# Performance work log

Hardware: AMD Instinct MI355X
Metric: run time of the kernel (lower is better)

Reference implementation:

```python
import jax, jax.numpy as jnp
import numpy as np

BATCH = 16384
D_MODEL = 2048
N_EXPERT = 64


def setup_inputs() -> dict:
    key = jax.random.key(0)
    kx, kw = jax.random.split(key)
    x = jax.random.normal(kx, (BATCH, D_MODEL), dtype=jnp.float32)
    # nn.Linear(d_model, n_expert, bias=False) -> weight [n_expert, d_model]
    w_gate = jax.random.normal(kw, (N_EXPERT, D_MODEL), dtype=jnp.float32) * (1.0 / np.sqrt(D_MODEL))
    return {"x": x, "w_gate": w_gate}


def reference(x, w_gate):
    # logits = x @ W^T : [batch, n_expert]
    logits = jnp.einsum("bd,ed->be", x, w_gate)
    idx = jnp.argmax(logits, axis=-1)                       # [batch]
    mask = jax.nn.one_hot(idx, logits.shape[-1], dtype=jnp.float32)  # [batch, nE]
    scores = jnp.sum(mask * logits, axis=-1, keepdims=True)  # [batch, 1]
    return (idx, scores, mask)
```

## Files before the change

kernel.cpp:

```cpp
#include <hip/hip_runtime.h>


typedef float  f32x4  __attribute__((ext_vector_type(4)));
typedef short  bf16x8 __attribute__((ext_vector_type(8)));

constexpr int BATCH = 16384;
constexpr int DM    = 2048;
constexpr int NE    = 64;
constexpr int BM    = 32;
constexpr int NT    = 256;


__device__ __forceinline__ void split_bf16(float f, unsigned short& hi, unsigned short& lo) {
    unsigned u  = __float_as_uint(f);
    unsigned h  = (u + 0x8000u) >> 16;
    float    hf = __uint_as_float(h << 16);
    unsigned l  = __float_as_uint(f - hf) >> 16;
    hi = (unsigned short)h;
    lo = (unsigned short)l;
}

__global__ __launch_bounds__(256, 1)
void wconv_kernel(const float* __restrict__ w, unsigned short* __restrict__ wf) {
    int i  = blockIdx.x * 256 + threadIdx.x;
    int ks = i >> 11;
    int n  = (i >> 9) & 3;
    int l  = (i >> 3) & 63;
    int j  = i & 7;
    int e  = n * 16 + (l & 15);
    int k  = ks * 32 + (l >> 4) * 8 + j;
    float v = w[(size_t)e * DM + k];
    unsigned short hi, lo;
    split_bf16(v, hi, lo);
    int base = ((ks * 2 + 0) * 4 + n) * 512 + l * 8 + j;
    wf[base]        = hi;
    wf[base + 2048] = lo;
}

struct BSet  { bf16x8 v[8]; };
struct BPair { BSet a, b; };

#define WAITV(N) do { asm volatile("s_waitcnt vmcnt(" #N ")" ::: "memory"); \
                      __builtin_amdgcn_sched_barrier(0); } while (0)
#define BARR     do { __builtin_amdgcn_sched_barrier(0); \
                      __builtin_amdgcn_s_barrier(); \
                      __builtin_amdgcn_sched_barrier(0); } while (0)

__global__ __launch_bounds__(NT, 2)
void gate_kernel(const float* __restrict__ x,
                 const unsigned short* __restrict__ wf,
                 float* __restrict__ out) {
    __shared__ alignas(16) float xs[4][16 * 64 * 4];
    __shared__ float lg[BM][NE + 1];
    __shared__ int   s_idx[BM];

    const int t     = threadIdx.x;
    const int lane  = t & 63;
    const int q     = t >> 6;
    const int row0  = blockIdx.x * BM;
    const int phase = blockIdx.x & 7;

    f32x4 acc[2][4];
    #pragma unroll
    for (int h = 0; h < 2; ++h)
        #pragma unroll
        for (int n = 0; n < 4; ++n) acc[h][n] = (f32x4){0.f, 0.f, 0.f, 0.f};

    auto sph = [&](int ss) { return (ss + phase) & 7; };

    auto stage_x = [&](int c) {
        const int h = c & 1;
        const float* xg = x + (size_t)(row0 + h * 16) * DM + sph(c >> 1) * 256;
        float* dst = &xs[c & 3][0];
        #pragma unroll
        for (int i = 0; i < 4; ++i) {
            int d  = i * NT + t;
            int r  = d >> 6;
            int sd = d & 63;
            int sr = sd ^ (r & 7);
            __builtin_amdgcn_global_load_lds(
                (const __attribute__((address_space(1))) void*)(xg + (size_t)r * DM + sr * 4),
                (__attribute__((address_space(3))) void*)(dst + d * 4),
                16, 0, 0);
        }
    };

    auto load_bs = [&](int ks, BSet& B) {
        const unsigned short* wg = wf + (size_t)ks * 4096 + lane * 8;
        #pragma unroll
        for (int f = 0; f < 8; ++f)
            B.v[f] = *(const bf16x8*)(wg + (size_t)f * 512);
    };
    auto load_pair = [&](int ss, BPair& P) {
        int base = sph(ss) * 8 + q * 2;
        load_bs(base + 0, P.a);
        load_bs(base + 1, P.b);
    };

    auto compute = [&](int c, int hh, const BPair& P) {
        const float* src = &xs[c & 3][0];
        const int rA = lane & 15;
        const int xr = rA & 7;
        #pragma unroll
        for (int kk = 0; kk < 2; ++kk) {
            const BSet& B = kk ? P.b : P.a;
            const int c0 = q * 16 + kk * 8 + ((lane >> 4) << 1);
            f32x4 a0 = *(const f32x4*)(src + (rA * 64 + ((c0 + 0) ^ xr)) * 4);
            f32x4 a1 = *(const f32x4*)(src + (rA * 64 + ((c0 + 1) ^ xr)) * 4);
            bf16x8 ahi, alo;
            #pragma unroll
            for (int j = 0; j < 8; ++j) {
                float f = (j < 4) ? a0[j] : a1[j - 4];
                unsigned short h, l;
                split_bf16(f, h, l);
                ahi[j] = (short)h;
                alo[j] = (short)l;
            }
            #pragma unroll
            for (int n = 0; n < 4; ++n) {
                acc[hh][n] = __builtin_amdgcn_mfma_f32_16x16x32_bf16(ahi, B.v[0 + n], acc[hh][n], 0, 0, 0);
                acc[hh][n] = __builtin_amdgcn_mfma_f32_16x16x32_bf16(ahi, B.v[4 + n], acc[hh][n], 0, 0, 0);
                acc[hh][n] = __builtin_amdgcn_mfma_f32_16x16x32_bf16(alo, B.v[0 + n], acc[hh][n], 0, 0, 0);
            }
        }
    };

    BPair PA, PB;

    load_pair(0, PA);
    stage_x(0);
    stage_x(1);

    #pragma unroll 1
    for (int ss = 0; ss < 6; ss += 2) {
        const int c = 2 * ss;
        load_pair(ss + 1, PB);
        stage_x(c + 2);
        WAITV(24); BARR;
        compute(c + 0, 0, PA);
        stage_x(c + 3);
        WAITV(24); BARR;
        compute(c + 1, 1, PA);
        load_pair(ss + 2, PA);
        stage_x(c + 4);
        WAITV(24); BARR;
        compute(c + 2, 0, PB);
        stage_x(c + 5);
        WAITV(24); BARR;
        compute(c + 3, 1, PB);
    }
    load_pair(7, PB);
    stage_x(14);
    WAITV(24); BARR;
    compute(12, 0, PA);
    stage_x(15);
    WAITV(24); BARR;
    compute(13, 1, PA);
    WAITV(4);  BARR;
    compute(14, 0, PB);
    WAITV(0);  BARR;
    compute(15, 1, PB);
    __syncthreads();

    const int rb = (lane >> 4) << 2;
    const int cb = lane & 15;
    if (q == 0) {
        #pragma unroll
        for (int h = 0; h < 2; ++h)
            #pragma unroll
            for (int n = 0; n < 4; ++n)
                #pragma unroll
                for (int j = 0; j < 4; ++j)
                    lg[h * 16 + rb + j][n * 16 + cb] = acc[h][n][j];
    }
    __syncthreads();
    if (q == 1) {
        #pragma unroll
        for (int h = 0; h < 2; ++h)
            #pragma unroll
            for (int n = 0; n < 4; ++n)
                #pragma unroll
                for (int j = 0; j < 4; ++j)
                    lg[h * 16 + rb + j][n * 16 + cb] += acc[h][n][j];
    }
    __syncthreads();
    if (q == 2) {
        #pragma unroll
        for (int h = 0; h < 2; ++h)
            #pragma unroll
            for (int n = 0; n < 4; ++n)
                #pragma unroll
                for (int j = 0; j < 4; ++j)
                    lg[h * 16 + rb + j][n * 16 + cb] += acc[h][n][j];
    }
    __syncthreads();
    if (q == 3) {
        #pragma unroll
        for (int h = 0; h < 2; ++h)
            #pragma unroll
            for (int n = 0; n < 4; ++n)
                #pragma unroll
                for (int j = 0; j < 4; ++j)
                    lg[h * 16 + rb + j][n * 16 + cb] += acc[h][n][j];
    }
    __syncthreads();

    if (t < BM) {
        float m  = lg[t][0];
        int   mi = 0;
        #pragma unroll
        for (int e = 1; e < NE; ++e) {
            float v = lg[t][e];
            if (v > m) { m = v; mi = e; }
        }
        s_idx[t] = mi;
        out[row0 + t]         = (float)mi;
        out[BATCH + row0 + t] = m;
    }
    __syncthreads();

    float* mask = out + 2 * (size_t)BATCH;
    int r  = t >> 3;
    int c0 = (t & 7) * 8;
    int mi = s_idx[r];
    #pragma unroll
    for (int i = 0; i < 2; ++i) {
        f32x4 v;
        #pragma unroll
        for (int j = 0; j < 4; ++j) v[j] = (c0 + i * 4 + j == mi) ? 1.0f : 0.0f;
        *(f32x4*)&mask[(size_t)(row0 + r) * NE + c0 + i * 4] = v;
    }
}

extern "C" void kernel_launch(void* const* d_in, const int* in_sizes, int n_in,
                              void* d_out, int out_size, void* d_ws, size_t ws_size,
                              hipStream_t stream) {
    const float* x = (const float*)d_in[0];
    const float* w = (const float*)d_in[1];
    float* out     = (float*)d_out;
    unsigned short* wf = (unsigned short*)d_ws;

    wconv_kernel<<<dim3(512), dim3(256), 0, stream>>>(w, wf);
    gate_kernel<<<dim3(BATCH / BM), dim3(NT), 0, stream>>>(x, wf, out);
}
```

Before: 43.65 us.

## Fuse weight bf16 split into gate kernel via LDS staging of fp32 weights

Drops the separate weight-conversion kernel and launch. Each block now streams fp32 weight tiles into LDS with async global-to-LDS loads and does the hi/lo bf16 split in registers before the MFMAs. The K step is halved to 128 and the pipeline is rebuilt around 16 stages with weight and x staging per pair. The cost is redundant weight conversion in every block, extra LDS traffic, and more barriers per K step.

```diff
diff --git a/kernel.cpp b/kernel.cpp
--- a/kernel.cpp
+++ b/kernel.cpp
@@ -9,7 +9,6 @@
 constexpr int NE    = 64;
 constexpr int BM    = 32;
 constexpr int NT    = 256;
-
 
 __device__ __forceinline__ void split_bf16(float f, unsigned short& hi, unsigned short& lo) {
     unsigned u  = __float_as_uint(f);
@@ -20,25 +19,7 @@
     lo = (unsigned short)l;
 }
 
-__global__ __launch_bounds__(256, 1)
-void wconv_kernel(const float* __restrict__ w, unsigned short* __restrict__ wf) {
-    int i  = blockIdx.x * 256 + threadIdx.x;
-    int ks = i >> 11;
-    int n  = (i >> 9) & 3;
-    int l  = (i >> 3) & 63;
-    int j  = i & 7;
-    int e  = n * 16 + (l & 15);
-    int k  = ks * 32 + (l >> 4) * 8 + j;
-    float v = w[(size_t)e * DM + k];
-    unsigned short hi, lo;
-    split_bf16(v, hi, lo);
-    int base = ((ks * 2 + 0) * 4 + n) * 512 + l * 8 + j;
-    wf[base]        = hi;
-    wf[base + 2048] = lo;
-}
-
-struct BSet  { bf16x8 v[8]; };
-struct BPair { BSet a, b; };
+struct BSet { bf16x8 v[8]; };
 
 #define WAITV(N) do { asm volatile("s_waitcnt vmcnt(" #N ")" ::: "memory"); \
                       __builtin_amdgcn_sched_barrier(0); } while (0)
@@ -48,9 +29,10 @@
 
 __global__ __launch_bounds__(NT, 2)
 void gate_kernel(const float* __restrict__ x,
-                 const unsigned short* __restrict__ wf,
+                 const float* __restrict__ w,
                  float* __restrict__ out) {
-    __shared__ alignas(16) float xs[4][16 * 64 * 4];
+    __shared__ alignas(16) float xs[4][16 * 32 * 4];
+    __shared__ alignas(16) float ws4[64 * 32 * 4];
     __shared__ float lg[BM][NE + 1];
     __shared__ int   s_idx[BM];
 
@@ -58,7 +40,7 @@
     const int lane  = t & 63;
     const int q     = t >> 6;
     const int row0  = blockIdx.x * BM;
-    const int phase = blockIdx.x & 7;
+    const int phase = blockIdx.x & 15;
 
     f32x4 acc[2][4];
     #pragma unroll
@@ -66,17 +48,17 @@
         #pragma unroll
         for (int n = 0; n < 4; ++n) acc[h][n] = (f32x4){0.f, 0.f, 0.f, 0.f};
 
-    auto sph = [&](int ss) { return (ss + phase) & 7; };
+    auto kb = [&](int p) { return (p + phase) & 15; };
 
     auto stage_x = [&](int c) {
         const int h = c & 1;
-        const float* xg = x + (size_t)(row0 + h * 16) * DM + sph(c >> 1) * 256;
+        const float* xg = x + (size_t)(row0 + h * 16) * DM + kb(c >> 1) * 128;
         float* dst = &xs[c & 3][0];
         #pragma unroll
-        for (int i = 0; i < 4; ++i) {
+        for (int i = 0; i < 2; ++i) {
             int d  = i * NT + t;
-            int r  = d >> 6;
-            int sd = d & 63;
+            int r  = d >> 5;
+            int sd = d & 31;
             int sr = sd ^ (r & 7);
             __builtin_amdgcn_global_load_lds(
                 (const __attribute__((address_space(1))) void*)(xg + (size_t)r * DM + sr * 4),
@@ -85,81 +67,93 @@
         }
     };
 
-    auto load_bs = [&](int ks, BSet& B) {
-        const unsigned short* wg = wf + (size_t)ks * 4096 + lane * 8;
-        #pragma unroll
-        for (int f = 0; f < 8; ++f)
-            B.v[f] = *(const bf16x8*)(wg + (size_t)f * 512);
-    };
-    auto load_pair = [&](int ss, BPair& P) {
-        int base = sph(ss) * 8 + q * 2;
-        load_bs(base + 0, P.a);
-        load_bs(base + 1, P.b);
-    };
-
-    auto compute = [&](int c, int hh, const BPair& P) {
+    auto stage_w = [&](int p) {
+        const float* wg = w + (size_t)kb(p) * 128;
+        #pragma unroll
+        for (int i = 0; i < 8; ++i) {
+            int d  = i * NT + t;
+            int e  = d >> 5;
+            int sd = d & 31;
+            int sr = sd ^ (e & 7);
+            __builtin_amdgcn_global_load_lds(
+                (const __attribute__((address_space(1))) void*)(wg + (size_t)e * DM + sr * 4),
+                (__attribute__((address_space(3))) void*)(ws4 + d * 4),
+                16, 0, 0);
+        }
+    };
+
+    auto compute = [&](int c, int hh, const BSet& B) {
         const float* src = &xs[c & 3][0];
         const int rA = lane & 15;
-        const int xr = rA & 7;
-        #pragma unroll
-        for (int kk = 0; kk < 2; ++kk) {
-            const BSet& B = kk ? P.b : P.a;
-            const int c0 = q * 16 + kk * 8 + ((lane >> 4) << 1);
-            f32x4 a0 = *(const f32x4*)(src + (rA * 64 + ((c0 + 0) ^ xr)) * 4);
-            f32x4 a1 = *(const f32x4*)(src + (rA * 64 + ((c0 + 1) ^ xr)) * 4);
-            bf16x8 ahi, alo;
+        const int s0 = q * 8 + ((lane >> 4) << 1);
+        f32x4 a0 = *(const f32x4*)(src + (size_t)(rA * 32 + ((s0 + 0) ^ (rA & 7))) * 4);
+        f32x4 a1 = *(const f32x4*)(src + (size_t)(rA * 32 + ((s0 + 1) ^ (rA & 7))) * 4);
+        bf16x8 ahi, alo;
+        #pragma unroll
+        for (int j = 0; j < 8; ++j) {
+            float f = (j < 4) ? a0[j] : a1[j - 4];
+            unsigned short h, l;
+            split_bf16(f, h, l);
+            ahi[j] = (short)h;
+            alo[j] = (short)l;
+        }
+        #pragma unroll
+        for (int n = 0; n < 4; ++n) {
+            acc[hh][n] = __builtin_amdgcn_mfma_f32_16x16x32_bf16(ahi, B.v[0 + n], acc[hh][n], 0, 0, 0);
+            acc[hh][n] = __builtin_amdgcn_mfma_f32_16x16x32_bf16(ahi, B.v[4 + n], acc[hh][n], 0, 0, 0);
+            acc[hh][n] = __builtin_amdgcn_mfma_f32_16x16x32_bf16(alo, B.v[0 + n], acc[hh][n], 0, 0, 0);
+        }
+    };
+
+    auto pairbody = [&](int p) {
+        BSet S;
+        #pragma unroll
+        for (int n = 0; n < 4; ++n) {
+            const int e  = n * 16 + (lane & 15);
+            const int s0 = q * 8 + ((lane >> 4) << 1);
+            f32x4 w0 = *(const f32x4*)&ws4[(size_t)(e * 32 + ((s0 + 0) ^ (e & 7))) * 4];
+            f32x4 w1 = *(const f32x4*)&ws4[(size_t)(e * 32 + ((s0 + 1) ^ (e & 7))) * 4];
+            bf16x8 hi8, lo8;
             #pragma unroll
             for (int j = 0; j < 8; ++j) {
-                float f = (j < 4) ? a0[j] : a1[j - 4];
+                float f = (j < 4) ? w0[j] : w1[j - 4];
                 unsigned short h, l;
                 split_bf16(f, h, l);
-                ahi[j] = (short)h;
-                alo[j] = (short)l;
+                hi8[j] = (short)h;
+                lo8[j] = (short)l;
             }
-            #pragma unroll
-            for (int n = 0; n < 4; ++n) {
-                acc[hh][n] = __builtin_amdgcn_mfma_f32_16x16x32_bf16(ahi, B.v[0 + n], acc[hh][n], 0, 0, 0);
-                acc[hh][n] = __builtin_amdgcn_mfma_f32_16x16x32_bf16(ahi, B.v[4 + n], acc[hh][n], 0, 0, 0);
-                acc[hh][n] = __builtin_amdgcn_mfma_f32_16x16x32_bf16(alo, B.v[0 + n], acc[hh][n], 0, 0, 0);
-            }
-        }
-    };
-
-    BPair PA, PB;
-
-    load_pair(0, PA);
+            S.v[n]     = hi8;
+            S.v[4 + n] = lo8;
+        }
+        compute(2 * p + 0, 0, S);
+        compute(2 * p + 1, 1, S);
+    };
+
     stage_x(0);
     stage_x(1);
+    stage_w(0);
+    stage_x(2);
+    stage_x(3);
+    WAITV(4);
+    BARR;
+    pairbody(0);
 
     #pragma unroll 1
-    for (int ss = 0; ss < 6; ss += 2) {
-        const int c = 2 * ss;
-        load_pair(ss + 1, PB);
-        stage_x(c + 2);
-        WAITV(24); BARR;
-        compute(c + 0, 0, PA);
-        stage_x(c + 3);
-        WAITV(24); BARR;
-        compute(c + 1, 1, PA);
-        load_pair(ss + 2, PA);
-        stage_x(c + 4);
-        WAITV(24); BARR;
-        compute(c + 2, 0, PB);
-        stage_x(c + 5);
-        WAITV(24); BARR;
-        compute(c + 3, 1, PB);
-    }
-    load_pair(7, PB);
-    stage_x(14);
-    WAITV(24); BARR;
-    compute(12, 0, PA);
-    stage_x(15);
-    WAITV(24); BARR;
-    compute(13, 1, PA);
-    WAITV(4);  BARR;
-    compute(14, 0, PB);
-    WAITV(0);  BARR;
-    compute(15, 1, PB);
+    for (int p = 1; p < 15; ++p) {
+        BARR;
+        stage_w(p);
+        stage_x(2 * p + 2);
+        stage_x(2 * p + 3);
+        WAITV(4);
+        BARR;
+        pairbody(p);
+    }
+
+    BARR;
+    stage_w(15);
+    WAITV(0);
+    BARR;
+    pairbody(15);
     __syncthreads();
 
     const int rb = (lane >> 4) << 2;
@@ -238,8 +232,6 @@
     const float* x = (const float*)d_in[0];
     const float* w = (const float*)d_in[1];
     float* out     = (float*)d_out;
-    unsigned short* wf = (unsigned short*)d_ws;
-
-    wconv_kernel<<<dim3(512), dim3(256), 0, stream>>>(w, wf);
-    gate_kernel<<<dim3(BATCH / BM), dim3(NT), 0, stream>>>(x, wf, out);
+
+    gate_kernel<<<dim3(BATCH / BM), dim3(NT), 0, stream>>>(x, w, out);
 }
```

Measured after the change: 38.56 us. 1.13x faster.

## Stage gate weights through LDS and double the row tile to 64

Applied to the files above, without the earlier changes.

The block tile grows to 64 rows with 512 threads. Each of the two row-tiles of waves splits K four ways. The bf16 hi/lo weight slab is now copied into LDS with global_load_lds and shared by all waves, instead of each wave holding B fragments in registers from global loads. The pipeline becomes a simple double-buffered loop over 16 K-chunks, each staging both x and the weights. The aim is to halve weight traffic per row and cut register pressure, at the cost of fewer resident blocks, extra LDS reads for B and a barrier-heavy two-stage pipeline.

```diff
diff --git a/kernel.cpp b/kernel.cpp
--- a/kernel.cpp
+++ b/kernel.cpp
@@ -7,8 +7,9 @@
 constexpr int BATCH = 16384;
 constexpr int DM    = 2048;
 constexpr int NE    = 64;
-constexpr int BM    = 32;
-constexpr int NT    = 256;
+constexpr int BM    = 64;
+constexpr int NT    = 512;
+constexpr int NCH   = 16;
 
 
 __device__ __forceinline__ void split_bf16(float f, unsigned short& hi, unsigned short& lo) {
@@ -37,46 +38,45 @@
     wf[base + 2048] = lo;
 }
 
-struct BSet  { bf16x8 v[8]; };
-struct BPair { BSet a, b; };
-
 #define WAITV(N) do { asm volatile("s_waitcnt vmcnt(" #N ")" ::: "memory"); \
                       __builtin_amdgcn_sched_barrier(0); } while (0)
 #define BARR     do { __builtin_amdgcn_sched_barrier(0); \
                       __builtin_amdgcn_s_barrier(); \
                       __builtin_amdgcn_sched_barrier(0); } while (0)
 
-__global__ __launch_bounds__(NT, 2)
+__global__ __launch_bounds__(NT, 1)
 void gate_kernel(const float* __restrict__ x,
                  const unsigned short* __restrict__ wf,
                  float* __restrict__ out) {
-    __shared__ alignas(16) float xs[4][16 * 64 * 4];
+    __shared__ alignas(16) float          xs[2][BM * 32 * 4];
+    __shared__ alignas(16) unsigned short bs[2][4 * 4096];
     __shared__ float lg[BM][NE + 1];
     __shared__ int   s_idx[BM];
 
     const int t     = threadIdx.x;
     const int lane  = t & 63;
-    const int q     = t >> 6;
+    const int wv    = t >> 6;
+    const int rt    = wv >> 2;
+    const int q     = wv & 3;
     const int row0  = blockIdx.x * BM;
-    const int phase = blockIdx.x & 7;
+    const int phase = blockIdx.x & 15;
 
     f32x4 acc[2][4];
     #pragma unroll
-    for (int h = 0; h < 2; ++h)
-        #pragma unroll
-        for (int n = 0; n < 4; ++n) acc[h][n] = (f32x4){0.f, 0.f, 0.f, 0.f};
-
-    auto sph = [&](int ss) { return (ss + phase) & 7; };
+    for (int s = 0; s < 2; ++s)
+        #pragma unroll
+        for (int n = 0; n < 4; ++n) acc[s][n] = (f32x4){0.f, 0.f, 0.f, 0.f};
+
+    auto ckOf = [&](int c) { return (c + phase) & 15; };
 
     auto stage_x = [&](int c) {
-        const int h = c & 1;
-        const float* xg = x + (size_t)(row0 + h * 16) * DM + sph(c >> 1) * 256;
-        float* dst = &xs[c & 3][0];
+        const float* xg = x + (size_t)row0 * DM + ckOf(c) * 128;
+        float* dst = &xs[c & 1][0];
         #pragma unroll
         for (int i = 0; i < 4; ++i) {
             int d  = i * NT + t;
-            int r  = d >> 6;
-            int sd = d & 63;
+            int r  = d >> 5;
+            int sd = d & 31;
             int sr = sd ^ (r & 7);
             __builtin_amdgcn_global_load_lds(
                 (const __attribute__((address_space(1))) void*)(xg + (size_t)r * DM + sr * 4),
@@ -85,28 +85,28 @@
         }
     };
 
-    auto load_bs = [&](int ks, BSet& B) {
-        const unsigned short* wg = wf + (size_t)ks * 4096 + lane * 8;
-        #pragma unroll
-        for (int f = 0; f < 8; ++f)
-            B.v[f] = *(const bf16x8*)(wg + (size_t)f * 512);
+    auto stage_b = [&](int c) {
+        const unsigned short* wg = wf + (size_t)ckOf(c) * 4 * 4096;
+        unsigned short* dst = &bs[c & 1][0];
+        #pragma unroll
+        for (int i = 0; i < 4; ++i) {
+            int d = i * NT + t;
+            __builtin_amdgcn_global_load_lds(
+                (const __attribute__((address_space(1))) void*)(wg + (size_t)d * 8),
+                (__attribute__((address_space(3))) void*)(dst + (size_t)d * 8),
+                16, 0, 0);
+        }
     };
-    auto load_pair = [&](int ss, BPair& P) {
-        int base = sph(ss) * 8 + q * 2;
-        load_bs(base + 0, P.a);
-        load_bs(base + 1, P.b);
-    };
-
-    auto compute = [&](int c, int hh, const BPair& P) {
-        const float* src = &xs[c & 3][0];
-        const int rA = lane & 15;
-        const int xr = rA & 7;
-        #pragma unroll
-        for (int kk = 0; kk < 2; ++kk) {
-            const BSet& B = kk ? P.b : P.a;
-            const int c0 = q * 16 + kk * 8 + ((lane >> 4) << 1);
-            f32x4 a0 = *(const f32x4*)(src + (rA * 64 + ((c0 + 0) ^ xr)) * 4);
-            f32x4 a1 = *(const f32x4*)(src + (rA * 64 + ((c0 + 1) ^ xr)) * 4);
+
+    auto compute = [&](int c) {
+        const float*          src  = &xs[c & 1][0];
+        const unsigned short* slab = &bs[c & 1][0];
+        #pragma unroll
+        for (int sub = 0; sub < 2; ++sub) {
+            const int row = rt * 32 + sub * 16 + (lane & 15);
+            const int s0  = q * 8 + ((lane >> 4) << 1);
+            f32x4 a0 = *(const f32x4*)(src + (size_t)(row * 32 + ((s0 + 0) ^ (row & 7))) * 4);
+            f32x4 a1 = *(const f32x4*)(src + (size_t)(row * 32 + ((s0 + 1) ^ (row & 7))) * 4);
             bf16x8 ahi, alo;
             #pragma unroll
             for (int j = 0; j < 8; ++j) {
@@ -118,90 +118,75 @@
             }
             #pragma unroll
             for (int n = 0; n < 4; ++n) {
-                acc[hh][n] = __builtin_amdgcn_mfma_f32_16x16x32_bf16(ahi, B.v[0 + n], acc[hh][n], 0, 0, 0);
-                acc[hh][n] = __builtin_amdgcn_mfma_f32_16x16x32_bf16(ahi, B.v[4 + n], acc[hh][n], 0, 0, 0);
-                acc[hh][n] = __builtin_amdgcn_mfma_f32_16x16x32_bf16(alo, B.v[0 + n], acc[hh][n], 0, 0, 0);
+                bf16x8 bhi = *(const bf16x8*)(slab + (size_t)q * 4096 + (0 * 4 + n) * 512 + lane * 8);
+                bf16x8 blo = *(const bf16x8*)(slab + (size_t)q * 4096 + (1 * 4 + n) * 512 + lane * 8);
+                acc[sub][n] = __builtin_amdgcn_mfma_f32_16x16x32_bf16(ahi, bhi, acc[sub][n], 0, 0, 0);
+                acc[sub][n] = __builtin_amdgcn_mfma_f32_16x16x32_bf16(ahi, blo, acc[sub][n], 0, 0, 0);
+                acc[sub][n] = __builtin_amdgcn_mfma_f32_16x16x32_bf16(alo, bhi, acc[sub][n], 0, 0, 0);
             }
         }
     };
 
-    BPair PA, PB;
-
-    load_pair(0, PA);
-    stage_x(0);
-    stage_x(1);
+    stage_x(0); stage_b(0);
+    stage_x(1); stage_b(1);
+    WAITV(8);
+    BARR;
 
     #pragma unroll 1
-    for (int ss = 0; ss < 6; ss += 2) {
-        const int c = 2 * ss;
-        load_pair(ss + 1, PB);
-        stage_x(c + 2);
-        WAITV(24); BARR;
-        compute(c + 0, 0, PA);
-        stage_x(c + 3);
-        WAITV(24); BARR;
-        compute(c + 1, 1, PA);
-        load_pair(ss + 2, PA);
-        stage_x(c + 4);
-        WAITV(24); BARR;
-        compute(c + 2, 0, PB);
-        stage_x(c + 5);
-        WAITV(24); BARR;
-        compute(c + 3, 1, PB);
-    }
-    load_pair(7, PB);
-    stage_x(14);
-    WAITV(24); BARR;
-    compute(12, 0, PA);
-    stage_x(15);
-    WAITV(24); BARR;
-    compute(13, 1, PA);
-    WAITV(4);  BARR;
-    compute(14, 0, PB);
-    WAITV(0);  BARR;
-    compute(15, 1, PB);
+    for (int c = 0; c < NCH - 2; ++c) {
+        compute(c);
+        BARR;
+        stage_x(c + 2); stage_b(c + 2);
+        WAITV(8);
+        BARR;
+    }
+    compute(NCH - 2);
+    BARR;
+    WAITV(0);
+    BARR;
+    compute(NCH - 1);
     __syncthreads();
 
     const int rb = (lane >> 4) << 2;
     const int cb = lane & 15;
     if (q == 0) {
         #pragma unroll
-        for (int h = 0; h < 2; ++h)
-            #pragma unroll
-            for (int n = 0; n < 4; ++n)
-                #pragma unroll
-                for (int j = 0; j < 4; ++j)
-                    lg[h * 16 + rb + j][n * 16 + cb] = acc[h][n][j];
+        for (int sub = 0; sub < 2; ++sub)
+            #pragma unroll
+            for (int n = 0; n < 4; ++n)
+                #pragma unroll
+                for (int j = 0; j < 4; ++j)
+                    lg[rt * 32 + sub * 16 + rb + j][n * 16 + cb] = acc[sub][n][j];
     }
     __syncthreads();
     if (q == 1) {
         #pragma unroll
-        for (int h = 0; h < 2; ++h)
-            #pragma unroll
-            for (int n = 0; n < 4; ++n)
-                #pragma unroll
-                for (int j = 0; j < 4; ++j)
-                    lg[h * 16 + rb + j][n * 16 + cb] += acc[h][n][j];
+        for (int sub = 0; sub < 2; ++sub)
+            #pragma unroll
+            for (int n = 0; n < 4; ++n)
+                #pragma unroll
+                for (int j = 0; j < 4; ++j)
+                    lg[rt * 32 + sub * 16 + rb + j][n * 16 + cb] += acc[sub][n][j];
     }
     __syncthreads();
     if (q == 2) {
         #pragma unroll
-        for (int h = 0; h < 2; ++h)
-            #pragma unroll
-            for (int n = 0; n < 4; ++n)
-                #pragma unroll
-                for (int j = 0; j < 4; ++j)
-                    lg[h * 16 + rb + j][n * 16 + cb] += acc[h][n][j];
+        for (int sub = 0; sub < 2; ++sub)
+            #pragma unroll
+            for (int n = 0; n < 4; ++n)
+                #pragma unroll
+                for (int j = 0; j < 4; ++j)
+                    lg[rt * 32 + sub * 16 + rb + j][n * 16 + cb] += acc[sub][n][j];
     }
     __syncthreads();
     if (q == 3) {
         #pragma unroll
-        for (int h = 0; h < 2; ++h)
-            #pragma unroll
-            for (int n = 0; n < 4; ++n)
-                #pragma unroll
-                for (int j = 0; j < 4; ++j)
-                    lg[h * 16 + rb + j][n * 16 + cb] += acc[h][n][j];
+        for (int sub = 0; sub < 2; ++sub)
+            #pragma unroll
+            for (int n = 0; n < 4; ++n)
+                #pragma unroll
+                for (int j = 0; j < 4; ++j)
+                    lg[rt * 32 + sub * 16 + rb + j][n * 16 + cb] += acc[sub][n][j];
     }
     __syncthreads();
 
```

New measurement: 44.35 us. About the same (+1.6%).
